# Kernel optimization log

Measured on AMD Instinct MI355X. Metric: run time of the kernel, lower is better.

## Reference

```python
import jax, jax.numpy as jnp
import numpy as np
from jax import lax

B, S, H, T = 64, 512, 1024, 17


def setup_inputs() -> dict:
    key = jax.random.key(0)
    ks = jax.random.split(key, 7)
    x = jax.random.normal(ks[0], (B, S, H), dtype=jnp.float32)
    W = jax.random.normal(ks[1], (T, H), dtype=jnp.float32) * 0.02
    b = jax.random.normal(ks[2], (T,), dtype=jnp.float32) * 0.02
    transitions = jax.random.normal(ks[3], (T, T), dtype=jnp.float32)
    start_trans = jax.random.normal(ks[4], (T,), dtype=jnp.float32)
    end_trans = jax.random.normal(ks[5], (T,), dtype=jnp.float32)
    nwords = jax.random.randint(ks[6], (B,), 1, S + 1, dtype=jnp.int32)
    return {"x": x, "W": W, "b": b, "transitions": transitions,
            "start_trans": start_trans, "end_trans": end_trans, "nwords": nwords}


def _viterbi(feats, mask_bs, transitions, start_trans, end_trans):
    # feats: [B,S,T]; mask_bs: [B,S] bool. Returns best tag sequence [B,S] (int32).
    Bt, St, Tt = feats.shape
    init = start_trans[None, :] + feats[:, 0]  # [B,T]
    idT = jnp.arange(Tt, dtype=jnp.int32)

    def step(score, inp):
        f_t, m_t = inp  # [B,T], [B]
        cand = score[:, :, None] + transitions[None, :, :]      # [B,Tprev,Tcur]
        best = jnp.max(cand, axis=1) + f_t                      # [B,T]
        bp = jnp.argmax(cand, axis=1).astype(jnp.int32)         # [B,T]
        m = m_t[:, None]
        new_score = jnp.where(m, best, score)
        bp = jnp.where(m, bp, idT[None, :])                     # identity where padded
        return new_score, bp

    xs = (jnp.swapaxes(feats[:, 1:], 0, 1), jnp.swapaxes(mask_bs[:, 1:], 0, 1))
    final, bps = lax.scan(step, init, xs)                       # bps: [S-1,B,T]
    final = final + end_trans[None, :]
    last_tag = jnp.argmax(final, axis=1).astype(jnp.int32)      # [B]

    def back(tag, bp_t):
        prev = jnp.take_along_axis(bp_t, tag[:, None], axis=1)[:, 0]
        return prev, tag

    first_tag, later_tags = lax.scan(back, last_tag, bps, reverse=True)
    tags = jnp.concatenate([first_tag[:, None], jnp.swapaxes(later_tags, 0, 1)], axis=1)  # [B,S]
    return tags


def reference(x, W, b, transitions, start_trans, end_trans, nwords):
    # dropout p=0.0 -> identity
    feats = jnp.einsum('bsh,th->bst', x, W) + b                 # hidden2tag
    mask_bs = jnp.arange(feats.shape[1])[None, :] < nwords[:, None]
    tags = _viterbi(feats, mask_bs, transitions, start_trans, end_trans)
    padded_tags = jnp.where(mask_bs, tags, 0).astype(jnp.float32)  # pad=0, float dtype
    return padded_tags, feats
```

## Files before the change

kernel.cpp:

```cpp
#include <hip/hip_runtime.h>

#define HDIM 1024
#define TDIM 17
#define BDIM 64
#define SDIM 512
#define NROWS (BDIM * SDIM)

__global__ __launch_bounds__(256) void gemm_kernel(
    const float* __restrict__ x, const float* __restrict__ W,
    const float* __restrict__ bias, float* __restrict__ feats) {
  __shared__ __align__(16) float sW[TDIM * 512];
  int tid = threadIdx.x;
  int sub = tid & 15;
  int g = tid >> 4;
  int row0 = blockIdx.x * 64 + g * 4;
  const float* xr = x + (size_t)row0 * HDIM;
  float acc[4][TDIM];
#pragma unroll
  for (int r = 0; r < 4; ++r)
#pragma unroll
    for (int t = 0; t < TDIM; ++t) acc[r][t] = 0.f;

  for (int ph = 0; ph < 2; ++ph) {
    if (ph) __syncthreads();
    for (int i = tid; i < TDIM * 128; i += 256) {
      int t = i >> 7;
      int k = (i & 127) * 4;
      *(float4*)&sW[t * 512 + k] =
          *(const float4*)&W[(size_t)t * HDIM + ph * 512 + k];
    }
    __syncthreads();
#pragma unroll
    for (int c = 0; c < 8; ++c) {
      float4 xv[4];
#pragma unroll
      for (int r = 0; r < 4; ++r)
        xv[r] = *(const float4*)(xr + r * HDIM + ph * 512 + c * 64 + sub * 4);
#pragma unroll
      for (int t = 0; t < TDIM; ++t) {
        float4 wv = *(const float4*)&sW[t * 512 + c * 64 + sub * 4];
#pragma unroll
        for (int r = 0; r < 4; ++r) {
          float a = acc[r][t];
          a = fmaf(xv[r].x, wv.x, a);
          a = fmaf(xv[r].y, wv.y, a);
          a = fmaf(xv[r].z, wv.z, a);
          a = fmaf(xv[r].w, wv.w, a);
          acc[r][t] = a;
        }
      }
    }
  }
#pragma unroll
  for (int r = 0; r < 4; ++r)
#pragma unroll
    for (int t = 0; t < TDIM; ++t) {
#pragma unroll
      for (int m = 1; m < 16; m <<= 1)
        acc[r][t] += __shfl_xor(acc[r][t], m, 64);
    }
#pragma unroll
  for (int r = 0; r < 4; ++r) {
    float val = acc[r][0];
#pragma unroll
    for (int t = 1; t < 16; ++t) val = (sub == t) ? acc[r][t] : val;
    feats[(size_t)(row0 + r) * TDIM + sub] = val + bias[sub];
    if (sub == 0)
      feats[(size_t)(row0 + r) * TDIM + 16] = acc[r][16] + bias[16];
  }
}

#define TRS 20
#define MVC 136

__global__ __launch_bounds__(64) void viterbi_kernel(
    const float* __restrict__ feats, const float* __restrict__ trans,
    const float* __restrict__ start_t, const float* __restrict__ end_t,
    const int* __restrict__ nwords, float* __restrict__ tags_out) {
  __shared__ __align__(16) float s_mv[64 * MVC];
  __shared__ float s_tr[TDIM * TRS];
  __shared__ unsigned char s_tags[SDIM];
  int b = blockIdx.x;
  int lane = threadIdx.x;
  const float* fb = feats + (size_t)b * SDIM * TDIM;

  for (int i = lane; i < TDIM * TDIM; i += 64)
    s_tr[(i / TDIM) * TRS + (i % TDIM)] = trans[i];
  __syncthreads();

  int nw = nwords[b];
  if (nw < 1) nw = 1;
  if (nw > SDIM) nw = SDIM;
  int jj = lane < TDIM ? lane : TDIM - 1;

  float tcol[TDIM];
#pragma unroll
  for (int i = 0; i < TDIM; ++i) tcol[i] = trans[i * TDIM + jj];

  float s[TDIM];
#pragma unroll
  for (int i = 0; i < TDIM; ++i) s[i] = start_t[i] + fb[i];
  float s0reg = start_t[jj] + fb[jj];

  auto load8g = [&](float* f, int t) {
#pragma unroll
    for (int u = 0; u < 8; ++u) f[u] = fb[(size_t)(t + u) * TDIM + jj];
  };

  auto step = [&](float fcu) -> float {
    float v[TDIM];
#pragma unroll
    for (int i = 0; i < TDIM; ++i) v[i] = s[i] + tcol[i];
    float m0 = fmaxf(fmaxf(v[0], v[1]), v[2]);
    float m1 = fmaxf(fmaxf(v[3], v[4]), v[5]);
    float m2 = fmaxf(fmaxf(v[6], v[7]), v[8]);
    float m3 = fmaxf(fmaxf(v[9], v[10]), v[11]);
    float m4 = fmaxf(fmaxf(v[12], v[13]), v[14]);
    float m5 = fmaxf(v[15], v[16]);
    float n0 = fmaxf(fmaxf(m0, m1), m2);
    float n1 = fmaxf(fmaxf(m3, m4), m5);
    float maxv = fmaxf(n0, n1);
    float ns = maxv + fcu;
#pragma unroll
    for (int i = 0; i < TDIM; ++i)
      s[i] = __uint_as_float(
          (unsigned)__builtin_amdgcn_readlane((int)__float_as_uint(ns), i));
    return maxv;
  };

  float fc[8], fn[8], mvr[8];
  load8g(fc, 0);
  {
    load8g(fn, 8);
    mvr[0] = 0.f;
#pragma unroll
    for (int u = 1; u < 8; ++u) {
      mvr[u] = 0.f;
      if (u < nw) mvr[u] = step(fc[u]);
    }
    if (lane < TDIM) {
      *(float4*)&s_mv[lane * 8] = make_float4(mvr[0], mvr[1], mvr[2], mvr[3]);
      *(float4*)&s_mv[lane * 8 + 4] =
          make_float4(mvr[4], mvr[5], mvr[6], mvr[7]);
    }
#pragma unroll
    for (int u = 0; u < 8; ++u) fc[u] = fn[u];
  }
  int t0 = 8;
  for (; t0 + 8 <= nw; t0 += 8) {
    int tn = (t0 + 8 <= SDIM - 8) ? t0 + 8 : t0;
    load8g(fn, tn);
#pragma unroll
    for (int u = 0; u < 8; ++u) mvr[u] = step(fc[u]);
    int cb = (t0 >> 3) * MVC;
    if (lane < TDIM) {
      *(float4*)&s_mv[cb + lane * 8] =
          make_float4(mvr[0], mvr[1], mvr[2], mvr[3]);
      *(float4*)&s_mv[cb + lane * 8 + 4] =
          make_float4(mvr[4], mvr[5], mvr[6], mvr[7]);
    }
#pragma unroll
    for (int u = 0; u < 8; ++u) fc[u] = fn[u];
  }
  if (t0 < nw) {
#pragma unroll
    for (int u = 0; u < 8; ++u) {
      mvr[u] = 0.f;
      if (t0 + u < nw) mvr[u] = step(fc[u]);
    }
    int cb = (t0 >> 3) * MVC;
    if (lane < TDIM) {
      *(float4*)&s_mv[cb + lane * 8] =
          make_float4(mvr[0], mvr[1], mvr[2], mvr[3]);
      *(float4*)&s_mv[cb + lane * 8 + 4] =
          make_float4(mvr[4], mvr[5], mvr[6], mvr[7]);
    }
  }

  float bv = s[0] + end_t[0];
  int bi = 0;
#pragma unroll
  for (int j = 1; j < TDIM; ++j) {
    float c = s[j] + end_t[j];
    bool p = c > bv;
    bv = p ? c : bv;
    bi = p ? j : bi;
  }
  int tag = __builtin_amdgcn_readfirstlane(bi);

  s_tags[nw - 1] = (unsigned char)tag;
  {
    int t = nw - 1;
    int ip = t - 1 > 0 ? t - 1 : 0;
    float fv = fb[(size_t)ip * TDIM + jj];
    float mvv = s_mv[(ip >> 3) * MVC + jj * 8 + (ip & 7)];
    while (t >= 1) {
      float tr = s_tr[jj * TRS + tag];
      float target = s_mv[(t >> 3) * MVC + tag * 8 + (t & 7)];
      int inx = t - 2 > 0 ? t - 2 : 0;
      float fvn = fb[(size_t)inx * TDIM + jj];
      float mvn = s_mv[(inx >> 3) * MVC + jj * 8 + (inx & 7)];
      float sv = (t - 1 == 0) ? s0reg : (mvv + fv);
      float cand = sv + tr;
      unsigned long long m = __ballot(cand == target) & 0x1FFFFull;
      tag = __ffsll(m) - 1;
      s_tags[t - 1] = (unsigned char)tag;
      fv = fvn;
      mvv = mvn;
      --t;
    }
  }
  __syncthreads();
  float* ob = tags_out + (size_t)b * SDIM;
  for (int t = lane; t < SDIM; t += 64)
    ob[t] = (t < nw) ? (float)s_tags[t] : 0.f;
}

extern "C" void kernel_launch(void* const* d_in, const int* in_sizes, int n_in,
                              void* d_out, int out_size, void* d_ws,
                              size_t ws_size, hipStream_t stream) {
  const float* x = (const float*)d_in[0];
  const float* W = (const float*)d_in[1];
  const float* b = (const float*)d_in[2];
  const float* trans = (const float*)d_in[3];
  const float* start_t = (const float*)d_in[4];
  const float* end_t = (const float*)d_in[5];
  const int* nwords = (const int*)d_in[6];
  float* out = (float*)d_out;
  float* tags_out = out;
  float* feats_out = out + NROWS;

  gemm_kernel<<<NROWS / 64, 256, 0, stream>>>(x, W, b, feats_out);
  viterbi_kernel<<<BDIM, 64, 0, stream>>>(feats_out, trans, start_t, end_t,
                                          nwords, tags_out);
}
```

Baseline: 338.6 us.

## Parallelize Viterbi over sequence chunks via max-plus chunk products and stitching

Replaces the single-block-per-batch sequential Viterbi with a four-kernel chunked scheme. Each 64-step chunk first computes its 17x17 max-plus transfer matrix in parallel. A short scan over chunk products gives the boundary scores, then each chunk is rerun from its boundary to record backpointers and per-end-tag paths, which a stitch kernel joins. This targets the long serial dependency chain of the Viterbi recurrence, at the cost of extra kernel launches, workspace traffic, a redundant rerun pass, and possible tie-break differences from max-plus reassociation.

```diff
diff --git a/kernel.cpp b/kernel.cpp
--- a/kernel.cpp
+++ b/kernel.cpp
@@ -5,6 +5,8 @@
 #define BDIM 64
 #define SDIM 512
 #define NROWS (BDIM * SDIM)
+#define NCH 8
+#define CHL 64
 
 __global__ __launch_bounds__(256) void gemm_kernel(
     const float* __restrict__ x, const float* __restrict__ W,
@@ -70,6 +72,203 @@
   }
 }
 
+__device__ __forceinline__ float vmax17(const float* v) {
+  float m0 = fmaxf(fmaxf(v[0], v[1]), v[2]);
+  float m1 = fmaxf(fmaxf(v[3], v[4]), v[5]);
+  float m2 = fmaxf(fmaxf(v[6], v[7]), v[8]);
+  float m3 = fmaxf(fmaxf(v[9], v[10]), v[11]);
+  float m4 = fmaxf(fmaxf(v[12], v[13]), v[14]);
+  float m5 = fmaxf(v[15], v[16]);
+  float n0 = fmaxf(fmaxf(m0, m1), m2);
+  float n1 = fmaxf(fmaxf(m3, m4), m5);
+  return fmaxf(n0, n1);
+}
+
+__global__ __launch_bounds__(384) void chunkprod_kernel(
+    const float* __restrict__ feats, const float* __restrict__ trans,
+    const int* __restrict__ nwords, float* __restrict__ Pbuf) {
+  int bc = blockIdx.x;
+  int b = bc >> 3, c = bc & 7;
+  int nw = nwords[b];
+  if (nw < 1) nw = 1;
+  if (nw > SDIM) nw = SDIM;
+  if (c > 0 && c * CHL > nw - 1) return;
+  int tid = threadIdx.x;
+  int wid = tid >> 6, lane = tid & 63;
+  int g = lane / 17, j = lane % 17;
+  int gc = g < 3 ? g : 2;
+  int e = wid * 3 + gc;
+  int ibase = gc * 17 * 4;
+  const float* fb = feats + (size_t)b * SDIM * TDIM;
+  float tcol[TDIM];
+#pragma unroll
+  for (int i = 0; i < TDIM; ++i) tcol[i] = trans[i * TDIM + j];
+  float s = (j == e) ? 0.f : -1e30f;
+  int t_start = (c == 0) ? 1 : c * CHL;
+  int t_end = c * CHL + CHL - 1;
+  if (t_end > nw - 1) t_end = nw - 1;
+  int tA = t_start;
+  int tB = t_start + 1;
+  if (tB > t_end) tB = t_start;
+  float fA = fb[(size_t)tA * TDIM + j];
+  float fB = fb[(size_t)tB * TDIM + j];
+  for (int t = t_start; t <= t_end; ++t) {
+    int t2 = t + 2;
+    if (t2 > t_end) t2 = t_end;
+    float fC = fb[(size_t)t2 * TDIM + j];
+    int sb = __float_as_int(s);
+    float v[TDIM];
+#pragma unroll
+    for (int i = 0; i < TDIM; ++i)
+      v[i] = __int_as_float(__builtin_amdgcn_ds_bpermute(ibase + 4 * i, sb)) +
+             tcol[i];
+    float maxv = vmax17(v);
+    s = maxv + fA;
+    fA = fB;
+    fB = fC;
+  }
+  if (g < 3 && e < TDIM)
+    Pbuf[((size_t)(b * NCH + c) * TDIM + e) * TDIM + j] = s;
+}
+
+__global__ __launch_bounds__(64) void scan_kernel(
+    const float* __restrict__ feats, const float* __restrict__ start_t,
+    const float* __restrict__ end_t, const int* __restrict__ nwords,
+    const float* __restrict__ Pbuf, float* __restrict__ bnd,
+    int* __restrict__ elast) {
+  int b = blockIdx.x;
+  int lane = threadIdx.x;
+  int jj = lane < TDIM ? lane : TDIM - 1;
+  int nw = nwords[b];
+  if (nw < 1) nw = 1;
+  if (nw > SDIM) nw = SDIM;
+  int clast = (nw - 1) >> 6;
+  float w = start_t[jj] + feats[(size_t)b * SDIM * TDIM + jj];
+  for (int c = 0; c <= clast; ++c) {
+    const float* Pc = Pbuf + (size_t)(b * NCH + c) * TDIM * TDIM;
+    float pj[TDIM];
+#pragma unroll
+    for (int i = 0; i < TDIM; ++i) pj[i] = Pc[i * TDIM + jj];
+    int wb = __float_as_int(w);
+    float v[TDIM];
+#pragma unroll
+    for (int i = 0; i < TDIM; ++i)
+      v[i] = __int_as_float(__builtin_amdgcn_ds_bpermute(4 * i, wb)) + pj[i];
+    w = vmax17(v);
+    if (lane < TDIM) bnd[(b * NCH + c) * TDIM + lane] = w;
+  }
+  float fin = w + end_t[jj];
+  float tmax = (lane < TDIM) ? fin : -1e30f;
+#pragma unroll
+  for (int m = 1; m < 64; m <<= 1) tmax = fmaxf(tmax, __shfl_xor(tmax, m, 64));
+  unsigned long long mm = __ballot(fin == tmax) & 0x1FFFFull;
+  if (lane == 0) elast[b] = (int)(__ffsll((unsigned long long)mm) - 1);
+}
+
+__global__ __launch_bounds__(64) void rerun_kernel(
+    const float* __restrict__ feats, const float* __restrict__ trans,
+    const float* __restrict__ start_t, const int* __restrict__ nwords,
+    const float* __restrict__ bnd, int* __restrict__ etag,
+    unsigned* __restrict__ seq32) {
+  __shared__ unsigned char s_bp[CHL * 20];
+  __shared__ __align__(4) unsigned char s_seq[TDIM * 68];
+  int bc = blockIdx.x;
+  int b = bc >> 3, c = bc & 7;
+  int nw = nwords[b];
+  if (nw < 1) nw = 1;
+  if (nw > SDIM) nw = SDIM;
+  if (c > 0 && c * CHL > nw - 1) return;
+  int lane = threadIdx.x;
+  int jj = lane < TDIM ? lane : TDIM - 1;
+  const float* fb = feats + (size_t)b * SDIM * TDIM;
+  float tcol[TDIM];
+#pragma unroll
+  for (int i = 0; i < TDIM; ++i) tcol[i] = trans[i * TDIM + jj];
+  float sj = (c == 0) ? (start_t[jj] + fb[jj])
+                      : bnd[(b * NCH + c - 1) * TDIM + jj];
+  int t_start = (c == 0) ? 1 : c * CHL;
+  int t_end = c * CHL + CHL - 1;
+  if (t_end > nw - 1) t_end = nw - 1;
+  int tA = t_start;
+  int tB = t_start + 1;
+  if (tB > t_end) tB = t_start;
+  float fA = fb[(size_t)tA * TDIM + jj];
+  float fB = fb[(size_t)tB * TDIM + jj];
+  for (int t = t_start; t <= t_end; ++t) {
+    int t2 = t + 2;
+    if (t2 > t_end) t2 = t_end;
+    float fC = fb[(size_t)t2 * TDIM + jj];
+    int sb = __float_as_int(sj);
+    float v[TDIM];
+#pragma unroll
+    for (int i = 0; i < TDIM; ++i)
+      v[i] = __int_as_float(__builtin_amdgcn_ds_bpermute(4 * i, sb)) + tcol[i];
+    float maxv = vmax17(v);
+    unsigned msk = 0;
+#pragma unroll
+    for (int i = 0; i < TDIM; ++i) msk |= (v[i] == maxv) ? (1u << i) : 0u;
+    int bp = __ffs(msk) - 1;
+    s_bp[(t - c * CHL) * 20 + jj] = (unsigned char)bp;
+    sj = maxv + fA;
+    fA = fB;
+    fB = fC;
+  }
+  __syncthreads();
+  if (lane < TDIM) {
+    int tag = lane;
+    for (int t = t_end; t >= t_start; --t) {
+      int u = t - c * CHL;
+      s_seq[lane * 68 + u] = (unsigned char)tag;
+      tag = s_bp[u * 20 + tag];
+    }
+    if (c == 0)
+      s_seq[lane * 68 + 0] = (unsigned char)tag;
+    else
+      etag[(b * NCH + c) * TDIM + lane] = tag;
+  }
+  __syncthreads();
+  for (int i = lane; i < TDIM * 16; i += 64) {
+    int e2 = i >> 4, q = i & 15;
+    seq32[(((size_t)(b * NCH + c) * TDIM + e2) << 4) + q] =
+        *(const unsigned*)&s_seq[e2 * 68 + q * 4];
+  }
+}
+
+__global__ __launch_bounds__(64) void stitch_kernel(
+    const int* __restrict__ nwords, const int* __restrict__ elast,
+    const int* __restrict__ etag, const unsigned* __restrict__ seq32,
+    float* __restrict__ tags_out) {
+  __shared__ unsigned long long stz[64];
+  int b = blockIdx.x;
+  int lane = threadIdx.x;
+  int nw = nwords[b];
+  if (nw < 1) nw = 1;
+  if (nw > SDIM) nw = SDIM;
+  stz[lane] = 0ull;
+  __syncthreads();
+  unsigned char* st = (unsigned char*)stz;
+  int clast = (nw - 1) >> 6;
+  int e = elast[b];
+  for (int c = clast; c >= 0; --c) {
+    int t_end = c * CHL + CHL - 1;
+    if (t_end > nw - 1) t_end = nw - 1;
+    int u_end = t_end - c * CHL;
+    if (lane < 16) {
+      unsigned wv = seq32[(((size_t)(b * NCH + c) * TDIM + e) << 4) + lane];
+#pragma unroll
+      for (int z = 0; z < 4; ++z) {
+        int u = lane * 4 + z;
+        if (u <= u_end) st[c * CHL + u] = (wv >> (8 * z)) & 0xff;
+      }
+    }
+    if (c > 0) e = etag[(b * NCH + c) * TDIM + e];
+  }
+  __syncthreads();
+  float* ob = tags_out + (size_t)b * SDIM;
+  for (int t = lane; t < SDIM; t += 64)
+    ob[t] = (t < nw) ? (float)st[t] : 0.f;
+}
+
 #define TRS 20
 #define MVC 136
 
@@ -83,43 +282,29 @@
   int b = blockIdx.x;
   int lane = threadIdx.x;
   const float* fb = feats + (size_t)b * SDIM * TDIM;
-
   for (int i = lane; i < TDIM * TDIM; i += 64)
     s_tr[(i / TDIM) * TRS + (i % TDIM)] = trans[i];
   __syncthreads();
-
   int nw = nwords[b];
   if (nw < 1) nw = 1;
   if (nw > SDIM) nw = SDIM;
   int jj = lane < TDIM ? lane : TDIM - 1;
-
   float tcol[TDIM];
 #pragma unroll
   for (int i = 0; i < TDIM; ++i) tcol[i] = trans[i * TDIM + jj];
-
   float s[TDIM];
 #pragma unroll
   for (int i = 0; i < TDIM; ++i) s[i] = start_t[i] + fb[i];
   float s0reg = start_t[jj] + fb[jj];
-
   auto load8g = [&](float* f, int t) {
 #pragma unroll
     for (int u = 0; u < 8; ++u) f[u] = fb[(size_t)(t + u) * TDIM + jj];
   };
-
   auto step = [&](float fcu) -> float {
     float v[TDIM];
 #pragma unroll
     for (int i = 0; i < TDIM; ++i) v[i] = s[i] + tcol[i];
-    float m0 = fmaxf(fmaxf(v[0], v[1]), v[2]);
-    float m1 = fmaxf(fmaxf(v[3], v[4]), v[5]);
-    float m2 = fmaxf(fmaxf(v[6], v[7]), v[8]);
-    float m3 = fmaxf(fmaxf(v[9], v[10]), v[11]);
-    float m4 = fmaxf(fmaxf(v[12], v[13]), v[14]);
-    float m5 = fmaxf(v[15], v[16]);
-    float n0 = fmaxf(fmaxf(m0, m1), m2);
-    float n1 = fmaxf(fmaxf(m3, m4), m5);
-    float maxv = fmaxf(n0, n1);
+    float maxv = vmax17(v);
     float ns = maxv + fcu;
 #pragma unroll
     for (int i = 0; i < TDIM; ++i)
@@ -127,7 +312,6 @@
           (unsigned)__builtin_amdgcn_readlane((int)__float_as_uint(ns), i));
     return maxv;
   };
-
   float fc[8], fn[8], mvr[8];
   load8g(fc, 0);
   {
@@ -176,18 +360,16 @@
           make_float4(mvr[4], mvr[5], mvr[6], mvr[7]);
     }
   }
-
   float bv = s[0] + end_t[0];
   int bi = 0;
 #pragma unroll
   for (int j = 1; j < TDIM; ++j) {
-    float c = s[j] + end_t[j];
-    bool p = c > bv;
-    bv = p ? c : bv;
+    float cc = s[j] + end_t[j];
+    bool p = cc > bv;
+    bv = p ? cc : bv;
     bi = p ? j : bi;
   }
   int tag = __builtin_amdgcn_readfirstlane(bi);
-
   s_tags[nw - 1] = (unsigned char)tag;
   {
     int t = nw - 1;
@@ -231,6 +413,24 @@
   float* feats_out = out + NROWS;
 
   gemm_kernel<<<NROWS / 64, 256, 0, stream>>>(x, W, b, feats_out);
-  viterbi_kernel<<<BDIM, 64, 0, stream>>>(feats_out, trans, start_t, end_t,
-                                          nwords, tags_out);
-}
+
+  if (ws_size >= (size_t)1218816 && d_ws != nullptr) {
+    char* ws = (char*)d_ws;
+    float* Pbuf = (float*)(ws);
+    float* bnd = (float*)(ws + 591872);
+    int* elast = (int*)(ws + 626688);
+    int* etag = (int*)(ws + 626944);
+    unsigned* seq32 = (unsigned*)(ws + 661760);
+    chunkprod_kernel<<<BDIM * NCH, 384, 0, stream>>>(feats_out, trans, nwords,
+                                                     Pbuf);
+    scan_kernel<<<BDIM, 64, 0, stream>>>(feats_out, start_t, end_t, nwords,
+                                         Pbuf, bnd, elast);
+    rerun_kernel<<<BDIM * NCH, 64, 0, stream>>>(feats_out, trans, start_t,
+                                                nwords, bnd, etag, seq32);
+    stitch_kernel<<<BDIM, 64, 0, stream>>>(nwords, elast, etag, seq32,
+                                           tags_out);
+  } else {
+    viterbi_kernel<<<BDIM, 64, 0, stream>>>(feats_out, trans, start_t, end_t,
+                                            nwords, tags_out);
+  }
+}
```

After: 296.3 us. 1.14x faster.
